# Performance work log

Measured on AMD Instinct MI355X. Metric: run time of the kernel, lower is better.

## Reference

```python
import jax, jax.numpy as jnp
import numpy as np

N, D, M1, K = 16384, 128, 64, 8  # batch, nodes (dims[0]), dims[1], k


def setup_inputs() -> dict:
    key = jax.random.key(0)
    ks = jax.random.split(key, 8)
    x = jax.random.normal(ks[0], (N, D), dtype=jnp.float32)
    # Stacked per-node fc1 weights: d independent Linear(d, m1) layers.
    s = 0.1
    w1_pos = jax.random.normal(ks[1], (D, M1, D), dtype=jnp.float32) * s
    b1_pos = jax.random.normal(ks[2], (D, M1), dtype=jnp.float32) * s
    w1_neg = jax.random.normal(ks[3], (D, M1, D), dtype=jnp.float32) * s
    b1_neg = jax.random.normal(ks[4], (D, M1), dtype=jnp.float32) * s
    # LocallyConnected(K, M1, 1): weight [K, M1, 1], bias [K, 1]
    w2 = jax.random.normal(ks[5], (K, M1, 1), dtype=jnp.float32) * s
    b2 = jax.random.normal(ks[6], (K, 1), dtype=jnp.float32) * s
    # fc3: d independent Linear(K, 1, bias=False) -> stacked [D, K]
    w3 = jax.random.normal(ks[7], (D, K), dtype=jnp.float32) * s
    return {"x": x, "w1_pos": w1_pos, "b1_pos": b1_pos,
            "w1_neg": w1_neg, "b1_neg": b1_neg,
            "w2": w2, "b2": b2, "w3": w3}


def reference(x, w1_pos, b1_pos, w1_neg, b1_neg, w2, b2, w3):
    d = x.shape[1]
    # Zeroing x[:, j] for node j == zeroing column j of node-j fc1 weight.
    mask = 1.0 - jnp.eye(d, dtype=x.dtype)            # [d, d]
    W = (w1_pos - w1_neg) * mask[:, None, :]          # [d, m1, d]
    b = b1_pos - b1_neg                                # [d, m1]
    h = jnp.einsum('nd,jmd->njm', x, W) + b            # [n, d, m1]
    # expand over K then sigmoid (sigmoid is identical for each k copy)
    h = jax.nn.sigmoid(h)
    # LocallyConnected: per-k matmul [m1 -> 1], bias [K, 1]
    z = jnp.einsum('njm,kmo->njko', h, w2) + b2        # [n, d, K, 1]
    z = z[..., 0]                                       # [n, d, K]
    # fc3: per-node Linear(K, 1, bias=False)
    out = jnp.einsum('njk,jk->nj', z, w3)              # [n, d]
    return out
```

## Files before the change

kernel.cpp:

```cpp
#include <hip/hip_runtime.h>
#include <hip/hip_bf16.h>

#define N_  16384
#define D_  128
#define M1_ 64
#define K_  8
#define LOG2E 1.44269504088896f

typedef short short8 __attribute__((ext_vector_type(8)));
typedef float f32x4  __attribute__((ext_vector_type(4)));

__device__ __forceinline__ ushort f2bf(float f) {
    union { float f; unsigned u; } un; un.f = f;
    unsigned u = un.u;
    return (ushort)((u + 0x7fffu + ((u >> 16) & 1u)) >> 16);
}

__global__ void prep_all(const float* __restrict__ x,
                         const float* __restrict__ w1p, const float* __restrict__ b1p,
                         const float* __restrict__ w1n, const float* __restrict__ b1n,
                         const float* __restrict__ w2,  const float* __restrict__ b2,
                         const float* __restrict__ w3,
                         ushort* __restrict__ xbf, ushort* __restrict__ wbf,
                         float* __restrict__ bp, float* __restrict__ vv,
                         float* __restrict__ cv) {
    int bx = blockIdx.x;
    if (bx < 2048) {
        int i = bx * 256 + threadIdx.x;
        int n = i >> 5;
        int d = (i & 31) * 4;
        float4 f = ((const float4*)x)[i];
        ushort4 o;
        o.x = f2bf(f.x); o.y = f2bf(f.y); o.z = f2bf(f.z); o.w = f2bf(f.w);
        int lane = (n & 15) + 16 * ((d >> 3) & 3);
        int idx  = (n >> 4) * 2048 + (d >> 5) * 512 + lane * 8 + (d & 7);
        *(ushort4*)&xbf[idx] = o;
    } else if (bx < 3072) {
        int i = (bx - 2048) * 256 + threadIdx.x;
        int base = i * 4;
        int j   = base >> 13;
        int rem = base & 8191;
        int m   = rem >> 7;
        int d   = rem & 127;
        float4 p = ((const float4*)w1p)[i];
        float4 n = ((const float4*)w1n)[i];
        float4 w;
        w.x = (p.x - n.x) * LOG2E; w.y = (p.y - n.y) * LOG2E;
        w.z = (p.z - n.z) * LOG2E; w.w = (p.w - n.w) * LOG2E;
        if (j == d    ) w.x = 0.f;
        if (j == d + 1) w.y = 0.f;
        if (j == d + 2) w.z = 0.f;
        if (j == d + 3) w.w = 0.f;
        ushort4 o;
        o.x = f2bf(w.x); o.y = f2bf(w.y); o.z = f2bf(w.z); o.w = f2bf(w.w);
        int lane = (m & 15) + 16 * ((d >> 3) & 3);
        int idx  = j * 8192 + ((d >> 5) * 4 + (m >> 4)) * 512 + lane * 8 + (d & 7);
        *(ushort4*)&wbf[idx] = o;
    } else {
        int idx = (bx - 3072) * 256 + threadIdx.x;
        int j = idx >> 6, m = idx & 63;
        float v = 0.f;
        for (int k = 0; k < K_; k++) v += w3[j * K_ + k] * w2[k * M1_ + m];
        vv[idx] = v;
        bp[idx] = (b1p[idx] - b1n[idx]) * LOG2E;
        if (m == 0) {
            float c = 0.f;
            for (int k = 0; k < K_; k++) c += w3[j * K_ + k] * b2[k];
            cv[j] = c;
        }
    }
}

__global__ __launch_bounds__(256) void main_mfma(
    const ushort* __restrict__ xbf, const ushort* __restrict__ wbf,
    const float* __restrict__ bvec, const float* __restrict__ vvec,
    const float* __restrict__ cvec, float* __restrict__ out) {
    const int tid  = threadIdx.x;
    const int wave = tid >> 6, lane = tid & 63;
    const int quad = lane >> 4, col = lane & 15;
    const int j    = blockIdx.y;
    const int nblk = blockIdx.x;

    short8 wfrag[4][4];
    const ushort* wg = wbf + (size_t)j * 8192 + lane * 8;
    #pragma unroll
    for (int ks = 0; ks < 4; ks++)
        #pragma unroll
        for (int mt = 0; mt < 4; mt++)
            wfrag[mt][ks] = *(const short8*)&wg[(ks * 4 + mt) * 512];

    f32x4 bias4[4], vm4[4];
    #pragma unroll
    for (int mt = 0; mt < 4; mt++) {
        bias4[mt] = *(const f32x4*)&bvec[j * M1_ + mt * 16 + quad * 4];
        vm4[mt]   = *(const f32x4*)&vvec[j * M1_ + mt * 16 + quad * 4];
    }
    const float cj = cvec[j];

    const ushort* xg = xbf + ((size_t)(nblk * 32 + wave)) * 2048 + lane * 8;
    float* outp = out + (size_t)(nblk * 512 + wave * 16 + col) * D_ + j;

    short8 abuf[2][4];
    #pragma unroll
    for (int ks = 0; ks < 4; ks++)
        abuf[0][ks] = *(const short8*)&xg[ks * 512];

    #pragma unroll 2
    for (int st = 0; st < 8; st++) {
        const int cur = st & 1, nxt = cur ^ 1;
        if (st < 7) {
            const ushort* xn = xg + (size_t)(st + 1) * 8192;
            #pragma unroll
            for (int ks = 0; ks < 4; ks++)
                abuf[nxt][ks] = *(const short8*)&xn[ks * 512];
        }

        f32x4 acc[4];
        #pragma unroll
        for (int mt = 0; mt < 4; mt++) acc[mt] = bias4[mt];
        #pragma unroll
        for (int ks = 0; ks < 4; ks++)
            #pragma unroll
            for (int mt = 0; mt < 4; mt++)
                acc[mt] = __builtin_amdgcn_mfma_f32_16x16x32_bf16(
                              wfrag[mt][ks], abuf[cur][ks], acc[mt], 0, 0, 0);

        float partial = 0.f;
        #pragma unroll
        for (int mt = 0; mt < 4; mt++)
            #pragma unroll
            for (int r = 0; r < 4; r++) {
                float e = __builtin_amdgcn_exp2f(-acc[mt][r]);
                float s = __builtin_amdgcn_rcpf(1.0f + e);
                partial = fmaf(s, vm4[mt][r], partial);
            }
        partial += __shfl_xor(partial, 16);
        partial += __shfl_xor(partial, 32);
        if (quad == 0)
            outp[(size_t)st * 64 * D_] = partial + cj;
    }
}

__global__ void fallback_kernel(const float* __restrict__ x,
                                const float* __restrict__ w1p, const float* __restrict__ b1p,
                                const float* __restrict__ w1n, const float* __restrict__ b1n,
                                const float* __restrict__ w2,  const float* __restrict__ b2,
                                const float* __restrict__ w3,  float* __restrict__ out) {
    int n = blockIdx.x, j = blockIdx.y, m = threadIdx.x;
    const float* xr = x + (size_t)n * D_;
    const float* wp = w1p + ((size_t)j * M1_ + m) * D_;
    const float* wn = w1n + ((size_t)j * M1_ + m) * D_;
    float acc = 0.f;
    for (int d = 0; d < D_; d++) {
        if (d == j) continue;
        acc += xr[d] * (wp[d] - wn[d]);
    }
    acc += b1p[j * M1_ + m] - b1n[j * M1_ + m];
    float h = 1.f / (1.f + __expf(-acc));
    float vmv = 0.f;
    for (int k = 0; k < K_; k++) vmv += w3[j * K_ + k] * w2[k * M1_ + m];
    float p = h * vmv;
    for (int off = 1; off < 64; off <<= 1) p += __shfl_xor(p, off);
    if (m == 0) {
        float c = 0.f;
        for (int k = 0; k < K_; k++) c += w3[j * K_ + k] * b2[k];
        out[(size_t)n * D_ + j] = p + c;
    }
}

extern "C" void kernel_launch(void* const* d_in, const int* in_sizes, int n_in,
                              void* d_out, int out_size, void* d_ws, size_t ws_size,
                              hipStream_t stream) {
    const float* x   = (const float*)d_in[0];
    const float* w1p = (const float*)d_in[1];
    const float* b1p = (const float*)d_in[2];
    const float* w1n = (const float*)d_in[3];
    const float* b1n = (const float*)d_in[4];
    const float* w2  = (const float*)d_in[5];
    const float* b2  = (const float*)d_in[6];
    const float* w3  = (const float*)d_in[7];
    float* out = (float*)d_out;

    const size_t off_x = 0;
    const size_t off_w = off_x + (size_t)N_ * D_ * 2;
    const size_t off_b = off_w + (size_t)D_ * M1_ * D_ * 2;
    const size_t off_v = off_b + (size_t)D_ * M1_ * 4;
    const size_t off_c = off_v + (size_t)D_ * M1_ * 4;
    const size_t need  = off_c + (size_t)D_ * 4;

    if (ws_size < need) {
        fallback_kernel<<<dim3(N_, D_), 64, 0, stream>>>(x, w1p, b1p, w1n, b1n, w2, b2, w3, out);
        return;
    }

    ushort* xbf = (ushort*)((char*)d_ws + off_x);
    ushort* wbf = (ushort*)((char*)d_ws + off_w);
    float*  bp  = (float*)((char*)d_ws + off_b);
    float*  vv  = (float*)((char*)d_ws + off_v);
    float*  cv  = (float*)((char*)d_ws + off_c);

    prep_all<<<3104, 256, 0, stream>>>(x, w1p, b1p, w1n, b1n, w2, b2, w3,
                                       xbf, wbf, bp, vv, cv);
    main_mfma<<<dim3(32, 128), 256, 0, stream>>>(xbf, wbf, bp, vv, cv, out);
}
```

Measured before the change: 124.5 us.

## Split M1 dimension across wave pairs with LDS reduction, double grid

Each block's four waves are now split into two M-halves and two N-groups, so each wave holds half the weight fragments and computes two 16-row M tiles instead of four. Partial sigmoid-weighted sums are combined across the M-halves through a small double-buffered LDS array with a block barrier, and the grid doubles to cover the rows. This cuts register pressure and increases the number of blocks, aiming for more occupancy and parallelism. The cost is a __syncthreads per step, each x tile being loaded by two waves, and fewer MFMAs per wave to hide latency.

Result: slower. 131.5 us (+5.6%).

```diff
diff --git a/kernel.cpp b/kernel.cpp
--- a/kernel.cpp
+++ b/kernel.cpp
@@ -75,69 +75,76 @@
     const ushort* __restrict__ xbf, const ushort* __restrict__ wbf,
     const float* __restrict__ bvec, const float* __restrict__ vvec,
     const float* __restrict__ cvec, float* __restrict__ out) {
+    __shared__ float ldsbuf[2][64];
     const int tid  = threadIdx.x;
     const int wave = tid >> 6, lane = tid & 63;
     const int quad = lane >> 4, col = lane & 15;
+    const int mhalf = wave >> 1, ngrp = wave & 1;
     const int j    = blockIdx.y;
     const int nblk = blockIdx.x;
 
-    short8 wfrag[4][4];
+    short8 wfrag[2][4];
     const ushort* wg = wbf + (size_t)j * 8192 + lane * 8;
     #pragma unroll
     for (int ks = 0; ks < 4; ks++)
         #pragma unroll
-        for (int mt = 0; mt < 4; mt++)
-            wfrag[mt][ks] = *(const short8*)&wg[(ks * 4 + mt) * 512];
-
-    f32x4 bias4[4], vm4[4];
-    #pragma unroll
-    for (int mt = 0; mt < 4; mt++) {
-        bias4[mt] = *(const f32x4*)&bvec[j * M1_ + mt * 16 + quad * 4];
-        vm4[mt]   = *(const f32x4*)&vvec[j * M1_ + mt * 16 + quad * 4];
+        for (int mtl = 0; mtl < 2; mtl++)
+            wfrag[mtl][ks] = *(const short8*)&wg[(ks * 4 + mhalf * 2 + mtl) * 512];
+
+    f32x4 bias4[2], vm4[2];
+    #pragma unroll
+    for (int mtl = 0; mtl < 2; mtl++) {
+        bias4[mtl] = *(const f32x4*)&bvec[j * M1_ + (mhalf * 2 + mtl) * 16 + quad * 4];
+        vm4[mtl]   = *(const f32x4*)&vvec[j * M1_ + (mhalf * 2 + mtl) * 16 + quad * 4];
     }
     const float cj = cvec[j];
 
-    const ushort* xg = xbf + ((size_t)(nblk * 32 + wave)) * 2048 + lane * 8;
-    float* outp = out + (size_t)(nblk * 512 + wave * 16 + col) * D_ + j;
+    const ushort* xg = xbf + ((size_t)(nblk * 16 + ngrp)) * 2048 + lane * 8;
+    float* outp = out + (size_t)(nblk * 256 + ngrp * 16 + col) * D_ + j;
 
     short8 abuf[2][4];
     #pragma unroll
     for (int ks = 0; ks < 4; ks++)
         abuf[0][ks] = *(const short8*)&xg[ks * 512];
 
-    #pragma unroll 2
+    #pragma unroll
     for (int st = 0; st < 8; st++) {
         const int cur = st & 1, nxt = cur ^ 1;
         if (st < 7) {
-            const ushort* xn = xg + (size_t)(st + 1) * 8192;
+            const ushort* xn = xg + (size_t)(st + 1) * 4096;
             #pragma unroll
             for (int ks = 0; ks < 4; ks++)
                 abuf[nxt][ks] = *(const short8*)&xn[ks * 512];
         }
 
-        f32x4 acc[4];
-        #pragma unroll
-        for (int mt = 0; mt < 4; mt++) acc[mt] = bias4[mt];
+        f32x4 acc[2];
+        #pragma unroll
+        for (int mtl = 0; mtl < 2; mtl++) acc[mtl] = bias4[mtl];
         #pragma unroll
         for (int ks = 0; ks < 4; ks++)
             #pragma unroll
-            for (int mt = 0; mt < 4; mt++)
-                acc[mt] = __builtin_amdgcn_mfma_f32_16x16x32_bf16(
-                              wfrag[mt][ks], abuf[cur][ks], acc[mt], 0, 0, 0);
+            for (int mtl = 0; mtl < 2; mtl++)
+                acc[mtl] = __builtin_amdgcn_mfma_f32_16x16x32_bf16(
+                               wfrag[mtl][ks], abuf[cur][ks], acc[mtl], 0, 0, 0);
 
         float partial = 0.f;
         #pragma unroll
-        for (int mt = 0; mt < 4; mt++)
+        for (int mtl = 0; mtl < 2; mtl++)
             #pragma unroll
             for (int r = 0; r < 4; r++) {
-                float e = __builtin_amdgcn_exp2f(-acc[mt][r]);
+                float e = __builtin_amdgcn_exp2f(-acc[mtl][r]);
                 float s = __builtin_amdgcn_rcpf(1.0f + e);
-                partial = fmaf(s, vm4[mt][r], partial);
+                partial = fmaf(s, vm4[mtl][r], partial);
             }
         partial += __shfl_xor(partial, 16);
         partial += __shfl_xor(partial, 32);
-        if (quad == 0)
-            outp[(size_t)st * 64 * D_] = partial + cj;
+
+        if (quad == 0) ldsbuf[cur][wave * 16 + col] = partial;
+        __syncthreads();
+        if (mhalf == 0 && quad == 0) {
+            float other = ldsbuf[cur][(wave + 2) * 16 + col];
+            outp[(size_t)st * 32 * D_] = partial + other + cj;
+        }
     }
 }
 
@@ -201,5 +208,5 @@
 
     prep_all<<<3104, 256, 0, stream>>>(x, w1p, b1p, w1n, b1n, w2, b2, w3,
                                        xbf, wbf, bp, vv, cv);
-    main_mfma<<<dim3(32, 128), 256, 0, stream>>>(xbf, wbf, bp, vv, cv, out);
-}
+    main_mfma<<<dim3(64, 128), 256, 0, stream>>>(xbf, wbf, bp, vv, cv, out);
+}
```
